# Optimization experiments

Hardware: AMD Instinct MI355X
Metric: run time of the kernel (lower is better)

Reference implementation:

```python
import jax, jax.numpy as jnp
import numpy as np

T, B, D, H, NQ = 512, 2048, 2, 64, 4


def setup_inputs() -> dict:
    key = jax.random.key(0)
    ks = jax.random.split(key, 16)
    f32 = jnp.float32
    seq = jax.random.normal(ks[0], (T, B, D), f32)
    s = 1.0 / np.sqrt(D + H)
    mk_w = lambda k: jax.random.uniform(k, (D + H, NQ), f32, -s, s)
    mk_b = lambda k: jax.random.uniform(k, (NQ,), f32, -s, s)
    mk_p = lambda k: jax.random.normal(k, (NQ,), f32)
    inp = dict(
        seq=seq,
        Wf=mk_w(ks[1]), bf=mk_b(ks[2]), pf=mk_p(ks[3]),
        Wi=mk_w(ks[4]), bi=mk_b(ks[5]), pi=mk_p(ks[6]),
        Wu=mk_w(ks[7]), bu=mk_b(ks[8]), pu=mk_p(ks[9]),
        Wo=mk_w(ks[10]), bo=mk_b(ks[11]), po=mk_p(ks[12]),
        Wc=jax.random.uniform(ks[13], (H, 1), f32, -1.0 / np.sqrt(H), 1.0 / np.sqrt(H)),
        bc=jax.random.uniform(ks[14], (1,), f32, -1.0 / np.sqrt(H), 1.0 / np.sqrt(H)),
    )
    return inp


def _qgate(z, p):
    # Analytic evaluation of the QGate circuit on |0..0>:
    #   RX(z_w) RX(p_w) on each wire, CNOT ring, <Z_0>.
    # Heisenberg picture: U^dag Z_0 U = Z_1 Z_2 ... Z_{NQ-1}, and on the
    # product state <Z_w> = cos(z_w + p_w), so the expval is
    #   prod_{w=1}^{NQ-1} cos(z_w + p_w)   (wire 0 cancels out).
    return jnp.prod(jnp.cos(z[:, 1:] + p[1:]), axis=1)  # (B,)


def reference(seq, Wf, bf, pf, Wi, bi, pi, Wu, bu, pu, Wo, bo, po, Wc, bc):
    Bn = seq.shape[1]
    Hn = Wc.shape[0]
    h0 = jnp.zeros((Bn, Hn), seq.dtype)

    def step(carry, x):
        hx, cx = carry
        comb = jnp.concatenate([x, hx], axis=1)  # (B, D+H)
        f = jax.nn.sigmoid(_qgate(comb @ Wf + bf, pf))[:, None]
        i = jax.nn.sigmoid(_qgate(comb @ Wi + bi, pi))[:, None]
        g = jnp.tanh(_qgate(comb @ Wu + bu, pu))[:, None]
        o = jax.nn.sigmoid(_qgate(comb @ Wo + bo, po))[:, None]
        cx = f * cx + i * g
        hx = o * jnp.tanh(cx)
        return (hx, cx), hx

    (_, _), outs = jax.lax.scan(step, (h0, h0), seq)  # outs: (T, B, H)
    # Original indexes lstm_out[:, -1, :] -> last batch element over all time.
    last = outs[:, -1, :]                 # (T, H)
    logits = last @ Wc + bc               # (T, 1)
    return jax.nn.sigmoid(logits)[:, 0]   # (T,)
```

## Files before the change

### kernel.cpp

```cpp
#include <hip/hip_runtime.h>

#define Tn 512
#define Bn 2048
#define Dn 2
#define NQn 4

#define INV2PI 0.15915494309189535f
#define L2E    1.4426950408889634f

__device__ __forceinline__ float fsig_hw(float x) {
    return __builtin_amdgcn_rcpf(1.f + __builtin_amdgcn_exp2f(-x * L2E));
}
__device__ __forceinline__ float ftanh_hw(float x) {
    return 1.f - 2.f * __builtin_amdgcn_rcpf(1.f + __builtin_amdgcn_exp2f(x * (2.f * L2E)));
}
template<int CTRL>
__device__ __forceinline__ float dppf(float x) {
    return __int_as_float(__builtin_amdgcn_mov_dpp(__float_as_int(x), CTRL, 0xF, 0xF, true));
}

__launch_bounds__(64)
__global__ void fraud_lstm_kernel(
    const float* __restrict__ seq,
    const float* __restrict__ Wf, const float* __restrict__ bf, const float* __restrict__ pf,
    const float* __restrict__ Wi, const float* __restrict__ bi, const float* __restrict__ pi,
    const float* __restrict__ Wu, const float* __restrict__ bu, const float* __restrict__ pu,
    const float* __restrict__ Wo, const float* __restrict__ bo, const float* __restrict__ po,
    const float* __restrict__ Wc, const float* __restrict__ bc,
    float* __restrict__ out)
{
    __shared__ float swArr[12], w0s[12], w1s[12], kqs[12];
    __shared__ float2 xs[Tn];
    __shared__ float zbuf[(Tn + 2) * 16];
    __shared__ float hbuf[Tn];
    __shared__ float sumWc;

    const int tid = threadIdx.x;
    const float* Wg[4] = {Wf, Wi, Wu, Wo};
    const float* bg[4] = {bf, bi, bu, bo};
    const float* pg[4] = {pf, pi, pu, po};

    for (int t = tid; t < Tn; t += 64) {
        const float* p = seq + (size_t)t * (Bn * Dn) + (size_t)(Bn - 1) * Dn;
        xs[t] = make_float2(p[0], p[1]);
    }

    #pragma unroll
    for (int m = 0; m < 12; ++m) {
        const int g = m / 3, q = 1 + (m % 3);
        float v = Wg[g][(Dn + tid) * NQn + q];
        #pragma unroll
        for (int off = 32; off > 0; off >>= 1) v += __shfl_down(v, off, 64);
        if (tid == 0) {
            swArr[m] = v * INV2PI;
            w0s[m]   = Wg[g][0 * NQn + q];
            w1s[m]   = Wg[g][1 * NQn + q];
            kqs[m]   = bg[g][q] + pg[g][q];
        }
    }
    {
        float v = Wc[tid];
        #pragma unroll
        for (int off = 32; off > 0; off >>= 1) v += __shfl_down(v, off, 64);
        if (tid == 0) sumWc = v;
    }
    __syncthreads();

    {
        const int m16 = tid & 15;
        const int g2 = m16 & 3, j2 = m16 >> 2;
        const int mm = g2 * 3 + j2;
        const bool live = (j2 < 3);
        const float w0 = live ? w0s[mm] : 0.f;
        const float w1 = live ? w1s[mm] : 0.f;
        const float kq = live ? kqs[mm] : 0.f;
        for (int t0 = (tid >> 4); t0 < Tn; t0 += 4) {
            const float2 x = xs[t0];
            zbuf[t0 * 16 + m16] = live ? fmaf(x.x, w0, fmaf(x.y, w1, kq)) * INV2PI : 0.f;
        }
    }
    __syncthreads();

    {
        const int l16 = tid & 15;
        const int g  = l16 & 3;
        const int jj = l16 >> 2;
        const float SWl = (jj < 3) ? swArr[g * 3 + jj] : 0.f;
        const bool isG2 = (g == 2);
        const float sscl = isG2 ? (2.f * L2E) : (-L2E);
        const float mulA = isG2 ? -2.f : 1.f;
        const float addA = isG2 ? 1.f : 0.f;

        float h = 0.f, c = 0.f;
        int zoff = l16;
        float zc = zbuf[zoff];
        float zn = zbuf[zoff + 16];
        float hsave = 0.f;

        for (int blk = 0; blk < 8; ++blk) {
            for (int t64 = 0; t64 < 64; ++t64) {
                const float zf = zbuf[zoff + 32];
                zoff += 16;
                const float z  = fmaf(h, SWl, zc);
                const float pc = __builtin_amdgcn_cosf(__builtin_amdgcn_fractf(z));
                const float p1  = pc * dppf<0x124>(pc);
                const float pre = p1 * dppf<0x128>(p1);
                const float r  = __builtin_amdgcn_rcpf(1.f + __builtin_amdgcn_exp2f(pre * sscl));
                const float A  = fmaf(mulA, r, addA);
                const float f  = dppf<0x00>(A);
                const float i  = dppf<0x55>(A);
                const float gu = dppf<0xAA>(A);
                const float o  = dppf<0xFF>(A);
                c = fmaf(f, c, i * gu);
                h = o * ftanh_hw(c);
                hsave = (tid == t64) ? h : hsave;
                zc = zn; zn = zf;
            }
            hbuf[blk * 64 + tid] = hsave;
        }
    }
    __syncthreads();

    const float swc = sumWc, b0 = bc[0];
    for (int t = tid; t < Tn; t += 64) {
        out[t] = fsig_hw(fmaf(hbuf[t], swc, b0));
    }
}

extern "C" void kernel_launch(void* const* d_in, const int* in_sizes, int n_in,
                              void* d_out, int out_size, void* d_ws, size_t ws_size,
                              hipStream_t stream) {
    const float* seq = (const float*)d_in[0];
    const float* Wf  = (const float*)d_in[1];
    const float* bf  = (const float*)d_in[2];
    const float* pf  = (const float*)d_in[3];
    const float* Wi  = (const float*)d_in[4];
    const float* bi  = (const float*)d_in[5];
    const float* pi  = (const float*)d_in[6];
    const float* Wu  = (const float*)d_in[7];
    const float* bu  = (const float*)d_in[8];
    const float* pu  = (const float*)d_in[9];
    const float* Wo  = (const float*)d_in[10];
    const float* bo  = (const float*)d_in[11];
    const float* po  = (const float*)d_in[12];
    const float* Wc  = (const float*)d_in[13];
    const float* bc  = (const float*)d_in[14];
    float* out = (float*)d_out;

    fraud_lstm_kernel<<<1, 64, 0, stream>>>(seq, Wf, bf, pf, Wi, bi, pi,
                                            Wu, bu, pu, Wo, bo, po, Wc, bc, out);
}
```

Measured before the change: 60.85 us.

## Replace transcendental gates with rational approximations and software-pipeline the recurrence

Swaps the exp/rcp-based sigmoid and tanh in the serial recurrence for Padé-style rational polynomials, which drops exp2 from the critical path and leaves one rcp per step for tanh. The h·SW product is folded into the next z value, so the loop carries only z. The loop is unrolled in blocks of 16 with double-buffered register prefetch of z from LDS. Instead of selecting h per lane, each step stores z to a new LDS buffer, and h is recovered afterwards by dividing by the largest-magnitude SW entry. This shortens the serial dependency chain at the cost of approximation accuracy and extra LDS use. Recovering h by division can also lose precision.

```diff
diff --git a/kernel.cpp b/kernel.cpp
--- a/kernel.cpp
+++ b/kernel.cpp
@@ -10,9 +10,6 @@
 
 __device__ __forceinline__ float fsig_hw(float x) {
     return __builtin_amdgcn_rcpf(1.f + __builtin_amdgcn_exp2f(-x * L2E));
-}
-__device__ __forceinline__ float ftanh_hw(float x) {
-    return 1.f - 2.f * __builtin_amdgcn_rcpf(1.f + __builtin_amdgcn_exp2f(x * (2.f * L2E)));
 }
 template<int CTRL>
 __device__ __forceinline__ float dppf(float x) {
@@ -31,8 +28,8 @@
 {
     __shared__ float swArr[12], w0s[12], w1s[12], kqs[12];
     __shared__ float2 xs[Tn];
-    __shared__ float zbuf[(Tn + 2) * 16];
-    __shared__ float hbuf[Tn];
+    __shared__ float zbuf[(Tn + 18) * 16];
+    __shared__ float zsbuf[Tn * 16 + 64];
     __shared__ float sumWc;
 
     const int tid = threadIdx.x;
@@ -78,6 +75,7 @@
             const float2 x = xs[t0];
             zbuf[t0 * 16 + m16] = live ? fmaf(x.x, w0, fmaf(x.y, w1, kq)) * INV2PI : 0.f;
         }
+        for (int i = tid; i < 18 * 16; i += 64) zbuf[Tn * 16 + i] = 0.f;
     }
     __syncthreads();
 
@@ -87,43 +85,85 @@
         const int jj = l16 >> 2;
         const float SWl = (jj < 3) ? swArr[g * 3 + jj] : 0.f;
         const bool isG2 = (g == 2);
-        const float sscl = isG2 ? (2.f * L2E) : (-L2E);
-        const float mulA = isG2 ? -2.f : 1.f;
-        const float addA = isG2 ? 1.f : 0.f;
+        const float cp0 = 945.f;
+        const float cp1 = isG2 ? 105.f : 26.25f;
+        const float cp2 = isG2 ? 1.f   : 0.0625f;
+        const float cq0 = isG2 ? 945.f : 3780.f;
+        const float cq1 = 420.f;
+        const float cq2 = isG2 ? 15.f  : 3.75f;
+        const float addA = isG2 ? 0.f  : 0.5f;
+        const float NA = isG2 ? 1.129352e-4f : 2.594063e-6f;
+        const float NB = isG2 ? -4.440815e-4f : -2.922584e-5f;
+        const float NC = isG2 ? 1.056778e-3f : 2.645420e-4f;
+        const float s0 = 10395.f * SWl, s1 = 1260.f * SWl, s2 = 21.f * SWl;
 
-        float h = 0.f, c = 0.f;
-        int zoff = l16;
-        float zc = zbuf[zoff];
-        float zn = zbuf[zoff + 16];
-        float hsave = 0.f;
+        float c = 0.f;
+        float zacc = zbuf[l16];
+        float za[16], zb2[16];
+        #pragma unroll
+        for (int k = 0; k < 16; ++k) za[k] = zbuf[(k + 1) * 16 + l16];
+        int ldoff = 17 * 16 + l16;
+        int woff = tid;
 
-        for (int blk = 0; blk < 8; ++blk) {
-            for (int t64 = 0; t64 < 64; ++t64) {
-                const float zf = zbuf[zoff + 32];
-                zoff += 16;
-                const float z  = fmaf(h, SWl, zc);
-                const float pc = __builtin_amdgcn_cosf(__builtin_amdgcn_fractf(z));
-                const float p1  = pc * dppf<0x124>(pc);
-                const float pre = p1 * dppf<0x128>(p1);
-                const float r  = __builtin_amdgcn_rcpf(1.f + __builtin_amdgcn_exp2f(pre * sscl));
-                const float A  = fmaf(mulA, r, addA);
-                const float f  = dppf<0x00>(A);
-                const float i  = dppf<0x55>(A);
-                const float gu = dppf<0xAA>(A);
-                const float o  = dppf<0xFF>(A);
-                c = fmaf(f, c, i * gu);
-                h = o * ftanh_hw(c);
-                hsave = (tid == t64) ? h : hsave;
-                zc = zn; zn = zf;
-            }
-            hbuf[blk * 64 + tid] = hsave;
+#define STEP(ZNV)                                                            \
+        {                                                                    \
+            const float pc  = __builtin_amdgcn_cosf(zacc);                   \
+            const float p1v = pc * dppf<0x124>(pc);                          \
+            const float u   = p1v * dppf<0x128>(p1v);                        \
+            const float w   = u * u;                                         \
+            const float Qd  = fmaf(w, fmaf(w, cq2, cq1), cq0);               \
+            const float r0  = fmaf(w, fmaf(w, NA, NB), NC);                  \
+            const float Pn  = fmaf(w, fmaf(w, cp2, cp1), cp0);               \
+            const float uPr = (u * Pn) * r0;                                 \
+            const float m1  = Qd * r0;                                       \
+            const float A   = fmaf(uPr, (2.f - m1), addA);                   \
+            const float fg  = dppf<0x00>(A);                                 \
+            const float ig  = dppf<0x55>(A);                                 \
+            const float gu  = dppf<0xAA>(A);                                 \
+            const float og  = dppf<0xFF>(A);                                 \
+            c = fmaf(fg, c, ig * gu);                                        \
+            const float y2   = c * c;                                        \
+            const float y2sq = y2 * y2;                                      \
+            const float oc   = og * c;                                       \
+            const float P2S  = fmaf(y2sq, s2, fmaf(y2, s1, s0));             \
+            const float Q2   = fmaf(y2sq, (y2 + 210.f), fmaf(y2, 4725.f, 10395.f)); \
+            const float rQ2  = __builtin_amdgcn_rcpf(Q2);                    \
+            zacc = fmaf(oc * P2S, rQ2, ZNV);                                 \
+            zsbuf[woff] = zacc;                                              \
+            woff += 16;                                                      \
         }
+
+        for (int sbp = 0; sbp < 16; ++sbp) {
+            #pragma unroll
+            for (int k = 0; k < 16; ++k) zb2[k] = zbuf[ldoff + k * 16];
+            #pragma unroll
+            for (int k = 0; k < 16; ++k) STEP(za[k]);
+            ldoff += 256;
+            #pragma unroll
+            for (int k = 0; k < 16; ++k) za[k] = zbuf[ldoff + k * 16];
+            #pragma unroll
+            for (int k = 0; k < 16; ++k) STEP(zb2[k]);
+            ldoff += 256;
+        }
+#undef STEP
     }
     __syncthreads();
 
-    const float swc = sumWc, b0 = bc[0];
-    for (int t = tid; t < Tn; t += 64) {
-        out[t] = fsig_hw(fmaf(hbuf[t], swc, b0));
+    {
+        int best = 0; float bv = 0.f;
+        #pragma unroll
+        for (int m = 0; m < 12; ++m) {
+            const float a = fabsf(swArr[m]);
+            if (a > bv) { bv = a; best = m; }
+        }
+        const int cbest = (best % 3) * 4 + (best / 3);
+        const float invSWb = 1.f / swArr[best];
+        const float swc = sumWc, b0 = bc[0];
+        for (int t = tid; t < Tn; t += 64) {
+            const float zs = zsbuf[t * 16 + cbest];
+            const float h  = (zs - zbuf[(t + 1) * 16 + cbest]) * invSWb;
+            out[t] = fsig_hw(fmaf(h, swc, b0));
+        }
     }
 }
 
```

New measurement: 57.25 us. 5.9% less time.

## Rewrite recurrence with product-to-sum cosines and rational sigmoid/tanh approximations

Applied to the files above, without the earlier changes.

Replaces the product of three cosines per gate with a sum of two cosines by folding the weights into sign-combined columns (product-to-sum identity). The sigmoid and tanh in the serial recurrence become Padé-style rational polynomials with a single reciprocal, and the exp/rcp pairs go away. Z inputs are prefetched into register double buffers, and each h value is written to LDS directly instead of through a per-lane select. The aim is a shorter serial dependency chain per timestep, with a risk of accuracy loss from the polynomial approximations and higher register pressure.

```diff
diff --git a/kernel.cpp b/kernel.cpp
--- a/kernel.cpp
+++ b/kernel.cpp
@@ -10,9 +10,6 @@
 
 __device__ __forceinline__ float fsig_hw(float x) {
     return __builtin_amdgcn_rcpf(1.f + __builtin_amdgcn_exp2f(-x * L2E));
-}
-__device__ __forceinline__ float ftanh_hw(float x) {
-    return 1.f - 2.f * __builtin_amdgcn_rcpf(1.f + __builtin_amdgcn_exp2f(x * (2.f * L2E)));
 }
 template<int CTRL>
 __device__ __forceinline__ float dppf(float x) {
@@ -30,9 +27,10 @@
     float* __restrict__ out)
 {
     __shared__ float swArr[12], w0s[12], w1s[12], kqs[12];
+    __shared__ float W0c[16], W1c[16], kqc[16];
     __shared__ float2 xs[Tn];
-    __shared__ float zbuf[(Tn + 2) * 16];
-    __shared__ float hbuf[Tn];
+    __shared__ float zbuf[(Tn + 18) * 16];
+    __shared__ float hbufx[Tn + 80];
     __shared__ float sumWc;
 
     const int tid = threadIdx.x;
@@ -66,64 +64,111 @@
     }
     __syncthreads();
 
-    {
-        const int m16 = tid & 15;
-        const int g2 = m16 & 3, j2 = m16 >> 2;
-        const int mm = g2 * 3 + j2;
-        const bool live = (j2 < 3);
-        const float w0 = live ? w0s[mm] : 0.f;
-        const float w1 = live ? w1s[mm] : 0.f;
-        const float kq = live ? kqs[mm] : 0.f;
-        for (int t0 = (tid >> 4); t0 < Tn; t0 += 4) {
-            const float2 x = xs[t0];
-            zbuf[t0 * 16 + m16] = live ? fmaf(x.x, w0, fmaf(x.y, w1, kq)) * INV2PI : 0.f;
-        }
+    if (tid < 16) {
+        const int col = tid, l8 = col >> 1, ab = col & 1;
+        const int g = l8 & 3, s2 = l8 >> 2;
+        const float sg0 = (s2 == 1 && ab == 1) ? -1.f : 1.f;
+        const float sg1 = (s2 == 1 && ab == 0) ? -1.f : 1.f;
+        const float sg2 = (s2 == 0 && ab == 1) ? -1.f : 1.f;
+        const int m = g * 3;
+        W0c[col] = sg0 * w0s[m] + sg1 * w0s[m + 1] + sg2 * w0s[m + 2];
+        W1c[col] = sg0 * w1s[m] + sg1 * w1s[m + 1] + sg2 * w1s[m + 2];
+        kqc[col] = sg0 * kqs[m] + sg1 * kqs[m + 1] + sg2 * kqs[m + 2];
     }
     __syncthreads();
 
     {
-        const int l16 = tid & 15;
-        const int g  = l16 & 3;
-        const int jj = l16 >> 2;
-        const float SWl = (jj < 3) ? swArr[g * 3 + jj] : 0.f;
+        const int col = tid & 15;
+        const float w0 = W0c[col], w1 = W1c[col], kq = kqc[col];
+        for (int t0 = (tid >> 4); t0 < Tn; t0 += 4) {
+            const float2 x = xs[t0];
+            zbuf[t0 * 16 + col] = fmaf(x.x, w0, fmaf(x.y, w1, kq)) * INV2PI;
+        }
+        for (int i = tid; i < 18 * 16; i += 64) zbuf[Tn * 16 + i] = 0.f;
+    }
+    __syncthreads();
+
+    {
+        const int l8 = tid & 7;
+        const int g  = l8 & 3;
+        const int s2 = l8 >> 2;
         const bool isG2 = (g == 2);
-        const float sscl = isG2 ? (2.f * L2E) : (-L2E);
-        const float mulA = isG2 ? -2.f : 1.f;
-        const float addA = isG2 ? 1.f : 0.f;
+        const int m = g * 3;
+        const float sw0 = swArr[m], sw1 = swArr[m + 1], sw2 = swArr[m + 2];
+        const float WAc = s2 ? (sw0 - sw1 + sw2) : (sw0 + sw1 + sw2);
+        const float WBc = s2 ? (-sw0 + sw1 + sw2) : (sw0 + sw1 - sw2);
+        const float cp0 = 236.25f;
+        const float cp1 = isG2 ? 1.640625f       : 0.41015625f;
+        const float cp2 = isG2 ? 9.765625e-4f    : 6.1035156e-5f;
+        const float cq0 = isG2 ? 945.f           : 3780.f;
+        const float cq1 = 26.25f;
+        const float cq2 = isG2 ? 5.859375e-2f    : 1.46484375e-2f;
+        const float addA = isG2 ? 0.f : 0.5f;
+        const float NA = isG2 ? 4.41153125e-7f  : 1.01330586e-8f;
+        const float NB = isG2 ? -2.77550938e-5f : -1.82661500e-6f;
+        const float NC = isG2 ? 1.056778e-3f    : 2.645420e-4f;
 
-        float h = 0.f, c = 0.f;
-        int zoff = l16;
-        float zc = zbuf[zoff];
-        float zn = zbuf[zoff + 16];
-        float hsave = 0.f;
+        const float2* zb2p = (const float2*)zbuf;
+        float c = 0.f;
+        float2 z0 = zb2p[l8];
+        float zaccA = z0.x, zaccB = z0.y;
+        float2 za2[16], zb2[16];
+        #pragma unroll
+        for (int k = 0; k < 16; ++k) za2[k] = zb2p[(k + 1) * 8 + l8];
+        int ldoff = 17 * 8 + l8;
+        int hidx  = (tid == 0) ? 0 : (Tn + 1 + tid);
+        const int hstep = (tid == 0) ? 1 : 0;
 
-        for (int blk = 0; blk < 8; ++blk) {
-            for (int t64 = 0; t64 < 64; ++t64) {
-                const float zf = zbuf[zoff + 32];
-                zoff += 16;
-                const float z  = fmaf(h, SWl, zc);
-                const float pc = __builtin_amdgcn_cosf(__builtin_amdgcn_fractf(z));
-                const float p1  = pc * dppf<0x124>(pc);
-                const float pre = p1 * dppf<0x128>(p1);
-                const float r  = __builtin_amdgcn_rcpf(1.f + __builtin_amdgcn_exp2f(pre * sscl));
-                const float A  = fmaf(mulA, r, addA);
-                const float f  = dppf<0x00>(A);
-                const float i  = dppf<0x55>(A);
-                const float gu = dppf<0xAA>(A);
-                const float o  = dppf<0xFF>(A);
-                c = fmaf(f, c, i * gu);
-                h = o * ftanh_hw(c);
-                hsave = (tid == t64) ? h : hsave;
-                zc = zn; zn = zf;
-            }
-            hbuf[blk * 64 + tid] = hsave;
+#define STEP(ZN2)                                                            \
+        {                                                                    \
+            const float cA = __builtin_amdgcn_cosf(zaccA);                   \
+            const float cB = __builtin_amdgcn_cosf(zaccB);                   \
+            const float sP = cA + cB;                                        \
+            const float s  = sP + dppf<0x124>(sP);                           \
+            const float w2 = s * s;                                          \
+            const float Qd = fmaf(w2, fmaf(w2, cq2, cq1), cq0);              \
+            const float r0 = fmaf(w2, fmaf(w2, NA, NB), NC);                 \
+            const float Pn = fmaf(w2, fmaf(w2, cp2, cp1), cp0);              \
+            const float uPr = (s * Pn) * r0;                                 \
+            const float m1 = Qd * r0;                                        \
+            const float A  = fmaf(uPr, (2.f - m1), addA);                    \
+            const float fg = dppf<0x00>(A);                                  \
+            const float ig = dppf<0x55>(A);                                  \
+            const float gu = dppf<0xAA>(A);                                  \
+            const float og = dppf<0xFF>(A);                                  \
+            c = fmaf(fg, c, ig * gu);                                        \
+            const float y  = c * c;                                          \
+            const float Q2 = fmaf(y, fmaf(y, (y + 210.f), 4725.f), 10395.f); \
+            const float rQ2 = __builtin_amdgcn_rcpf(Q2);                     \
+            const float P2 = fmaf(y, fmaf(y, 21.f, 1260.f), 10395.f);        \
+            const float ocP = (og * c) * P2;                                 \
+            const float kA = ocP * WAc;                                      \
+            const float kB = ocP * WBc;                                      \
+            zaccA = fmaf(kA, rQ2, (ZN2).x);                                  \
+            zaccB = fmaf(kB, rQ2, (ZN2).y);                                  \
+            hbufx[hidx] = ocP * rQ2;                                         \
+            hidx += hstep;                                                   \
         }
+
+        for (int sbp = 0; sbp < 16; ++sbp) {
+            #pragma unroll
+            for (int k = 0; k < 16; ++k) zb2[k] = zb2p[ldoff + k * 8];
+            #pragma unroll
+            for (int k = 0; k < 16; ++k) STEP(za2[k]);
+            ldoff += 128;
+            #pragma unroll
+            for (int k = 0; k < 16; ++k) za2[k] = zb2p[ldoff + k * 8];
+            #pragma unroll
+            for (int k = 0; k < 16; ++k) STEP(zb2[k]);
+            ldoff += 128;
+        }
+#undef STEP
     }
     __syncthreads();
 
     const float swc = sumWc, b0 = bc[0];
     for (int t = tid; t < Tn; t += 64) {
-        out[t] = fsig_hw(fmaf(hbuf[t], swc, b0));
+        out[t] = fsig_hw(fmaf(hbufx[t], swc, b0));
     }
 }
 
```

Measured after the change: 55.13 us. -9.4%, faster.
